# Performance work log

Hardware: AMD Instinct MI355X
Metric: run time of the kernel (lower is better)

## Reference

```python
import jax, jax.numpy as jnp
import numpy as np

# --- Instant-NGP hash grid hyperparameters ---
L = 12            # n_levels (multires)
T = 2 ** 19       # hash table size per level
F = 2             # features per level -> feature_dim = L*F = 24
BASE_RES = 16
MAX_RES = 2048
N_PTS = 524288
D_OUT = 257

_growth = np.exp((np.log(MAX_RES) - np.log(BASE_RES)) / (L - 1))
RES = np.floor(BASE_RES * _growth ** np.arange(L)).astype(np.int32)  # per-level grid resolution
PRIMES = jnp.array([1, 2654435761, 805459861], dtype=jnp.uint32)
# 8 corner offsets of a voxel, [8,3] in {0,1}
OFFS = np.array([[(i >> 2) & 1, (i >> 1) & 1, i & 1] for i in range(8)], dtype=np.int32)
OFFS_U32 = jnp.asarray(OFFS, dtype=jnp.uint32)
OFFS_BOOL = jnp.asarray(OFFS.astype(bool))


def hash_encode(x, tables):
    """x: [N,3] in [0,1]; tables: [L,T,F]. Returns [N, L*F]."""
    outs = []
    for l in range(L):
        pos = x * RES[l]                      # [N,3]
        p0 = jnp.floor(pos)
        frac = pos - p0                       # [N,3] trilinear fractions
        corners = p0.astype(jnp.uint32)[:, None, :] + OFFS_U32[None]  # [N,8,3]
        h = corners * PRIMES[None, None, :]   # uint32 wrap-around mult
        idx = (h[..., 0] ^ h[..., 1] ^ h[..., 2]) & jnp.uint32(T - 1)  # [N,8]
        feats = tables[l][idx.astype(jnp.int32)]                       # [N,8,F] gather
        # trilinear weights: prod over dims of frac or (1-frac)
        w = jnp.prod(jnp.where(OFFS_BOOL[None], frac[:, None, :], 1.0 - frac[:, None, :]), axis=-1)  # [N,8]
        # windowed_embed: coarse-to-fine window weight; alpha = L (fully trained) -> weight 1.0
        outs.append(jnp.einsum('nc,ncf->nf', w, feats))
    return jnp.concatenate(outs, axis=-1)     # [N, L*F]


def setup_inputs() -> dict:
    key = jax.random.key(0)
    k1, k2, k3 = jax.random.split(key, 3)
    inputs = jax.random.uniform(k1, (N_PTS, 3), dtype=jnp.float32)
    tables = jax.random.normal(k2, (L, T, F), dtype=jnp.float32) * 1e-2
    W = jax.random.normal(k3, (L * F, D_OUT), dtype=jnp.float32) * (1.0 / np.sqrt(L * F))
    bias = jnp.zeros((D_OUT,), dtype=jnp.float32)
    return {"inputs": inputs, "tables": tables, "W": W, "bias": bias}


def reference(inputs, tables, W, bias):
    emb = hash_encode(inputs, tables)          # [N, 24]
    y = emb @ W + bias                         # TCNNLinear head, [N, 257]
    # torch.cat([x[:, :1], x[:, 1:]], -1) is identity; keep for fidelity
    return jnp.concatenate([y[:, :1], y[:, 1:]], axis=-1)
```

## Files before the change

### kernel.cpp

```cpp
#include <hip/hip_runtime.h>
#include <math.h>

#define NLEV 12
#define TSIZE (1u << 19)
#define TMASK (TSIZE - 1u)
#define DOUT 257
#define PPB 256
#define EMB 24
#define RSTRIDE 28
#define TP 128
#define EPT 2
#define EPB (256 * EPT)

struct ResArr { float r[NLEV]; };

struct Corner { unsigned idx[8]; float w[8]; };

__device__ __forceinline__ void hash_corners(float rf, float px, float py, float pz,
                                             Corner& c)
{
    const float sx = px * rf, sy = py * rf, sz = pz * rf;
    const float gx = floorf(sx), gy = floorf(sy), gz = floorf(sz);
    const float tx = sx - gx, ty = sy - gy, tz = sz - gz;
    const unsigned ix = (unsigned)gx, iy = (unsigned)gy, iz = (unsigned)gz;
    const unsigned hx0 = ix,               hx1 = ix + 1u;
    const unsigned hy0 = iy * 2654435761u, hy1 = hy0 + 2654435761u;
    const unsigned hz0 = iz * 805459861u,  hz1 = hz0 + 805459861u;
    c.idx[0] = (hx0 ^ hy0 ^ hz0) & TMASK;
    c.idx[1] = (hx0 ^ hy0 ^ hz1) & TMASK;
    c.idx[2] = (hx0 ^ hy1 ^ hz0) & TMASK;
    c.idx[3] = (hx0 ^ hy1 ^ hz1) & TMASK;
    c.idx[4] = (hx1 ^ hy0 ^ hz0) & TMASK;
    c.idx[5] = (hx1 ^ hy0 ^ hz1) & TMASK;
    c.idx[6] = (hx1 ^ hy1 ^ hz0) & TMASK;
    c.idx[7] = (hx1 ^ hy1 ^ hz1) & TMASK;
    const float u0 = 1.0f - tx, u1 = tx;
    const float v0 = 1.0f - ty, v1 = ty;
    const float s0 = 1.0f - tz, s1 = tz;
    c.w[0] = (u0 * v0) * s0;
    c.w[1] = (u0 * v0) * s1;
    c.w[2] = (u0 * v1) * s0;
    c.w[3] = (u0 * v1) * s1;
    c.w[4] = (u1 * v0) * s0;
    c.w[5] = (u1 * v0) * s1;
    c.w[6] = (u1 * v1) * s0;
    c.w[7] = (u1 * v1) * s1;
}

__global__ __launch_bounds__(256)
void encode_kernel(const float* __restrict__ xin,
                   const float* __restrict__ tables,
                   float2* __restrict__ emb2,
                   int N, int nbpl, ResArr res)
{
    const int lvl = blockIdx.x / nbpl;
    const int bx  = blockIdx.x - lvl * nbpl;
    const int pA  = bx * EPB + threadIdx.x;
    const int pB  = pA + 256;
    if (pA >= N) return;
    const bool hasB = (pB < N);

    const float ax = xin[3 * pA + 0];
    const float ay = xin[3 * pA + 1];
    const float az = xin[3 * pA + 2];
    float bx_ = 0.f, by_ = 0.f, bz_ = 0.f;
    if (hasB) {
        bx_ = xin[3 * pB + 0];
        by_ = xin[3 * pB + 1];
        bz_ = xin[3 * pB + 2];
    }

    const float rf = res.r[lvl];
    Corner cA, cB;
    hash_corners(rf, ax, ay, az, cA);
    hash_corners(rf, bx_, by_, bz_, cB);

    const float2* __restrict__ tab = (const float2*)tables + (size_t)lvl * TSIZE;

    float2 fA[8], fB[8];
#pragma unroll
    for (int i = 0; i < 8; ++i) fA[i] = tab[cA.idx[i]];
#pragma unroll
    for (int i = 0; i < 8; ++i) fB[i] = tab[cB.idx[i]];

    float a = cA.w[0] * fA[0].x;
    float b = cA.w[0] * fA[0].y;
#pragma unroll
    for (int i = 1; i < 8; ++i) {
        a = fmaf(cA.w[i], fA[i].x, a);
        b = fmaf(cA.w[i], fA[i].y, b);
    }
    emb2[(size_t)lvl * N + pA] = make_float2(a, b);

    if (hasB) {
        float a2 = cB.w[0] * fB[0].x;
        float b2 = cB.w[0] * fB[0].y;
#pragma unroll
        for (int i = 1; i < 8; ++i) {
            a2 = fmaf(cB.w[i], fB[i].x, a2);
            b2 = fmaf(cB.w[i], fB[i].y, b2);
        }
        emb2[(size_t)lvl * N + pB] = make_float2(a2, b2);
    }
}

__global__ __launch_bounds__(256)
void head_kernel(const float2* __restrict__ emb2,
                 const float* __restrict__ Wm,
                 const float* __restrict__ bias,
                 float* __restrict__ out,
                 int N)
{
    __shared__ float2 sm[NLEV][TP];
    const int tid  = threadIdx.x;
    const int base = blockIdx.x * TP;
    const int nv   = min(TP, N - base);

    float wcol[EMB];
#pragma unroll
    for (int k = 0; k < EMB; ++k) wcol[k] = Wm[k * DOUT + tid];
    const float bj = bias[tid];

#pragma unroll
    for (int i = 0; i < (NLEV * TP) / 256; ++i) {
        const int f = i * 256 + tid;
        const int l = f >> 7;
        const int n = f & (TP - 1);
        if (n < nv) sm[l][n] = emb2[(size_t)l * N + base + n];
    }
    __syncthreads();

    float* orow = out + (size_t)base * DOUT + tid;
    for (int n = 0; n < nv; ++n, orow += DOUT) {
        float accA = bj, accB = 0.0f;
#pragma unroll
        for (int l = 0; l < NLEV; l += 2) {
            const float2 q0 = sm[l][n];
            const float2 q1 = sm[l + 1][n];
            accA = fmaf(q0.x, wcol[2 * l + 0], accA);
            accB = fmaf(q0.y, wcol[2 * l + 1], accB);
            accA = fmaf(q1.x, wcol[2 * l + 2], accA);
            accB = fmaf(q1.y, wcol[2 * l + 3], accB);
        }
        *orow = accA + accB;
    }

    if (tid < nv) {
        float acc = bias[256];
#pragma unroll
        for (int l = 0; l < NLEV; ++l) {
            const float2 q = sm[l][tid];
            acc = fmaf(q.x, Wm[(2 * l) * DOUT + 256],
                  fmaf(q.y, Wm[(2 * l + 1) * DOUT + 256], acc));
        }
        out[(size_t)(base + tid) * DOUT + 256] = acc;
    }
}

__global__ __launch_bounds__(256)
void hashgrid_head_kernel(const float* __restrict__ xin,
                          const float* __restrict__ tables,
                          const float* __restrict__ Wm,
                          const float* __restrict__ bias,
                          float* __restrict__ out,
                          int N, ResArr res)
{
    __shared__ float emb[PPB * RSTRIDE];
    const int tid  = threadIdx.x;
    const int base = blockIdx.x * PPB;
    const int p    = base + tid;

    float wcol[EMB];
#pragma unroll
    for (int k = 0; k < EMB; ++k) wcol[k] = Wm[k * DOUT + tid];
    const float bj = bias[tid];

    const bool extra = (tid < 64);
    float wext[EMB];
    float bext = 0.0f;
    if (extra) {
#pragma unroll
        for (int k = 0; k < EMB; ++k) wext[k] = Wm[k * DOUT + 256];
        bext = bias[256];
    }

    if (p < N) {
        const float px = xin[3 * p + 0];
        const float py = xin[3 * p + 1];
        const float pz = xin[3 * p + 2];
#pragma unroll 2
        for (int l = 0; l < NLEV; ++l) {
            const float rf = res.r[l];
            Corner c;
            hash_corners(rf, px, py, pz, c);
            const float2* __restrict__ tab = (const float2*)tables + (size_t)l * TSIZE;
            float2 f[8];
#pragma unroll
            for (int i = 0; i < 8; ++i) f[i] = tab[c.idx[i]];
            float a = c.w[0] * f[0].x;
            float b = c.w[0] * f[0].y;
#pragma unroll
            for (int i = 1; i < 8; ++i) {
                a = fmaf(c.w[i], f[i].x, a);
                b = fmaf(c.w[i], f[i].y, b);
            }
            *(float2*)&emb[tid * RSTRIDE + 2 * l] = make_float2(a, b);
        }
    }

    __syncthreads();

    const int nvalid = min(PPB, N - base);
    for (int n = 0; n < nvalid; ++n) {
        const float4* e4 = (const float4*)&emb[n * RSTRIDE];
        float4 q0 = e4[0], q1 = e4[1], q2 = e4[2], q3 = e4[3], q4 = e4[4], q5 = e4[5];
        float e[EMB] = {q0.x, q0.y, q0.z, q0.w, q1.x, q1.y, q1.z, q1.w,
                        q2.x, q2.y, q2.z, q2.w, q3.x, q3.y, q3.z, q3.w,
                        q4.x, q4.y, q4.z, q4.w, q5.x, q5.y, q5.z, q5.w};
        float acc = bj;
#pragma unroll
        for (int k = 0; k < EMB; ++k) acc = fmaf(e[k], wcol[k], acc);
        out[(size_t)(base + n) * DOUT + tid] = acc;
        if (extra) {
            float acc2 = bext;
#pragma unroll
            for (int k = 0; k < EMB; ++k) acc2 = fmaf(e[k], wext[k], acc2);
            if (tid == 0) out[(size_t)(base + n) * DOUT + 256] = acc2;
        }
    }
}

extern "C" void kernel_launch(void* const* d_in, const int* in_sizes, int n_in,
                              void* d_out, int out_size, void* d_ws, size_t ws_size,
                              hipStream_t stream) {
    const float* xin    = (const float*)d_in[0];
    const float* tables = (const float*)d_in[1];
    const float* Wm     = (const float*)d_in[2];
    const float* bias   = (const float*)d_in[3];
    float* out = (float*)d_out;
    const int N = in_sizes[0] / 3;

    ResArr res;
    const double growth = exp((log(2048.0) - log(16.0)) / 11.0);
    for (int l = 0; l < NLEV; ++l)
        res.r[l] = (float)floor(16.0 * pow(growth, (double)l));

    const size_t need = (size_t)NLEV * (size_t)N * sizeof(float2);
    if (d_ws != nullptr && ws_size >= need) {
        float2* emb2 = (float2*)d_ws;
        const int nbpl = (N + EPB - 1) / EPB;
        hipLaunchKernelGGL(encode_kernel, dim3(nbpl * NLEV), dim3(256), 0, stream,
                           xin, tables, emb2, N, nbpl, res);
        hipLaunchKernelGGL(head_kernel, dim3((N + TP - 1) / TP), dim3(256), 0, stream,
                           emb2, Wm, bias, out, N);
    } else {
        const int grid = (N + PPB - 1) / PPB;
        hipLaunchKernelGGL(hashgrid_head_kernel, dim3(grid), dim3(PPB), 0, stream,
                           xin, tables, Wm, bias, out, N, res);
    }
}
```

Before: 821.6 us.

## Restructure head kernel to wave-per-row with register-held weights; simplify encode to one point

The encode kernel drops from two points per thread to one point per thread and writes its embedding with nontemporal stores. The head kernel is reorganized so each wavefront computes a full output row. Every lane holds four output columns' weights in registers plus the 257th column, which folds the separate extra-column pass into the main loop. Output rows are written with nontemporal stores to avoid polluting cache with the large output. The trade-off is higher register pressure (about 125 weight registers), and the encode kernel loses the per-thread memory-level parallelism it had from handling two points.

```diff
diff --git a/kernel.cpp b/kernel.cpp
--- a/kernel.cpp
+++ b/kernel.cpp
@@ -9,10 +9,9 @@
 #define EMB 24
 #define RSTRIDE 28
 #define TP 128
-#define EPT 2
-#define EPB (256 * EPT)
 
 struct ResArr { float r[NLEV]; };
+typedef float __attribute__((ext_vector_type(2))) f32x2;
 
 struct Corner { unsigned idx[8]; float w[8]; };
 
@@ -55,53 +54,31 @@
 {
     const int lvl = blockIdx.x / nbpl;
     const int bx  = blockIdx.x - lvl * nbpl;
-    const int pA  = bx * EPB + threadIdx.x;
-    const int pB  = pA + 256;
-    if (pA >= N) return;
-    const bool hasB = (pB < N);
-
-    const float ax = xin[3 * pA + 0];
-    const float ay = xin[3 * pA + 1];
-    const float az = xin[3 * pA + 2];
-    float bx_ = 0.f, by_ = 0.f, bz_ = 0.f;
-    if (hasB) {
-        bx_ = xin[3 * pB + 0];
-        by_ = xin[3 * pB + 1];
-        bz_ = xin[3 * pB + 2];
-    }
+    const int p   = bx * 256 + threadIdx.x;
+    if (p >= N) return;
+
+    const float px = xin[3 * p + 0];
+    const float py = xin[3 * p + 1];
+    const float pz = xin[3 * p + 2];
 
     const float rf = res.r[lvl];
-    Corner cA, cB;
-    hash_corners(rf, ax, ay, az, cA);
-    hash_corners(rf, bx_, by_, bz_, cB);
+    Corner c;
+    hash_corners(rf, px, py, pz, c);
 
     const float2* __restrict__ tab = (const float2*)tables + (size_t)lvl * TSIZE;
-
-    float2 fA[8], fB[8];
-#pragma unroll
-    for (int i = 0; i < 8; ++i) fA[i] = tab[cA.idx[i]];
-#pragma unroll
-    for (int i = 0; i < 8; ++i) fB[i] = tab[cB.idx[i]];
-
-    float a = cA.w[0] * fA[0].x;
-    float b = cA.w[0] * fA[0].y;
+    float2 f[8];
+#pragma unroll
+    for (int i = 0; i < 8; ++i) f[i] = tab[c.idx[i]];
+
+    float a = c.w[0] * f[0].x;
+    float b = c.w[0] * f[0].y;
 #pragma unroll
     for (int i = 1; i < 8; ++i) {
-        a = fmaf(cA.w[i], fA[i].x, a);
-        b = fmaf(cA.w[i], fA[i].y, b);
-    }
-    emb2[(size_t)lvl * N + pA] = make_float2(a, b);
-
-    if (hasB) {
-        float a2 = cB.w[0] * fB[0].x;
-        float b2 = cB.w[0] * fB[0].y;
-#pragma unroll
-        for (int i = 1; i < 8; ++i) {
-            a2 = fmaf(cB.w[i], fB[i].x, a2);
-            b2 = fmaf(cB.w[i], fB[i].y, b2);
-        }
-        emb2[(size_t)lvl * N + pB] = make_float2(a2, b2);
-    }
+        a = fmaf(c.w[i], f[i].x, a);
+        b = fmaf(c.w[i], f[i].y, b);
+    }
+    f32x2 v; v.x = a; v.y = b;
+    __builtin_nontemporal_store(v, (f32x2*)(emb2 + (size_t)lvl * N + p));
 }
 
 __global__ __launch_bounds__(256)
@@ -113,13 +90,24 @@
 {
     __shared__ float2 sm[NLEV][TP];
     const int tid  = threadIdx.x;
+    const int lane = tid & 63;
+    const int wv   = tid >> 6;
     const int base = blockIdx.x * TP;
     const int nv   = min(TP, N - base);
 
-    float wcol[EMB];
-#pragma unroll
-    for (int k = 0; k < EMB; ++k) wcol[k] = Wm[k * DOUT + tid];
-    const float bj = bias[tid];
+    float wcol[EMB][4];
+    float wext[EMB];
+#pragma unroll
+    for (int k = 0; k < EMB; ++k) {
+#pragma unroll
+        for (int c = 0; c < 4; ++c)
+            wcol[k][c] = Wm[k * DOUT + 64 * c + lane];
+        wext[k] = Wm[k * DOUT + 256];
+    }
+    float bcol[4];
+#pragma unroll
+    for (int c = 0; c < 4; ++c) bcol[c] = bias[64 * c + lane];
+    const float b256 = bias[256];
 
 #pragma unroll
     for (int i = 0; i < (NLEV * TP) / 256; ++i) {
@@ -130,30 +118,29 @@
     }
     __syncthreads();
 
-    float* orow = out + (size_t)base * DOUT + tid;
-    for (int n = 0; n < nv; ++n, orow += DOUT) {
-        float accA = bj, accB = 0.0f;
-#pragma unroll
-        for (int l = 0; l < NLEV; l += 2) {
-            const float2 q0 = sm[l][n];
-            const float2 q1 = sm[l + 1][n];
-            accA = fmaf(q0.x, wcol[2 * l + 0], accA);
-            accB = fmaf(q0.y, wcol[2 * l + 1], accB);
-            accA = fmaf(q1.x, wcol[2 * l + 2], accA);
-            accB = fmaf(q1.y, wcol[2 * l + 3], accB);
-        }
-        *orow = accA + accB;
-    }
-
-    if (tid < nv) {
-        float acc = bias[256];
+    for (int n = wv; n < nv; n += 4) {
+        float e[EMB];
 #pragma unroll
         for (int l = 0; l < NLEV; ++l) {
-            const float2 q = sm[l][tid];
-            acc = fmaf(q.x, Wm[(2 * l) * DOUT + 256],
-                  fmaf(q.y, Wm[(2 * l + 1) * DOUT + 256], acc));
-        }
-        out[(size_t)(base + tid) * DOUT + 256] = acc;
+            const float2 q = sm[l][n];
+            e[2 * l]     = q.x;
+            e[2 * l + 1] = q.y;
+        }
+        float a0 = bcol[0], a1 = bcol[1], a2 = bcol[2], a3 = bcol[3], a4 = b256;
+#pragma unroll
+        for (int k = 0; k < EMB; ++k) {
+            a0 = fmaf(e[k], wcol[k][0], a0);
+            a1 = fmaf(e[k], wcol[k][1], a1);
+            a2 = fmaf(e[k], wcol[k][2], a2);
+            a3 = fmaf(e[k], wcol[k][3], a3);
+            a4 = fmaf(e[k], wext[k], a4);
+        }
+        float* orow = out + (size_t)(base + n) * DOUT;
+        __builtin_nontemporal_store(a0, orow + lane);
+        __builtin_nontemporal_store(a1, orow + 64 + lane);
+        __builtin_nontemporal_store(a2, orow + 128 + lane);
+        __builtin_nontemporal_store(a3, orow + 192 + lane);
+        if (lane == 0) __builtin_nontemporal_store(a4, orow + 256);
     }
 }
 
@@ -248,7 +235,7 @@
     const size_t need = (size_t)NLEV * (size_t)N * sizeof(float2);
     if (d_ws != nullptr && ws_size >= need) {
         float2* emb2 = (float2*)d_ws;
-        const int nbpl = (N + EPB - 1) / EPB;
+        const int nbpl = (N + 255) / 256;
         hipLaunchKernelGGL(encode_kernel, dim3(nbpl * NLEV), dim3(256), 0, stream,
                            xin, tables, emb2, N, nbpl, res);
         hipLaunchKernelGGL(head_kernel, dim3((N + TP - 1) / TP), dim3(256), 0, stream,
```

New measurement: 855.6 us. 1.04x slower.
